# Optimization experiments

Measured on AMD Instinct MI355X. Metric: run time of the kernel, lower is better.

The kernel has to match this reference:

```python
import jax, jax.numpy as jnp
import numpy as np

B, N, K, OUT = 8, 2048, 30, 13


def _knn_idx(x, k):
    # x: [B,N,F] -> indices of k nearest neighbors (squared L2, includes self)
    sq = jnp.sum(x * x, axis=-1)  # [B,N]
    d = sq[:, :, None] + sq[:, None, :] - 2.0 * jnp.einsum('bnf,bmf->bnm', x, x)
    _, idx = jax.lax.top_k(-d, k)  # [B,N,k]
    return idx


def _edge_conv(x, W1, b1, g, be, W2, b2, k):
    # DynamicEdgeConv: kNN on feature space, message = MLP([x_i, x_j - x_i]), max aggr
    idx = _knn_idx(x, k)                                  # [B,N,k] (non-differentiable)
    xj = jax.vmap(lambda xb, ib: xb[ib])(x, idx)          # gather neighbors [B,N,k,F]
    xi = x[:, :, None, :]
    e = jnp.concatenate([jnp.broadcast_to(xi, xj.shape), xj - xi], axis=-1)  # [B,N,k,2F]
    # PyG MLP([2F,64,64]): Linear + BN(eval: affine) + ReLU, then plain Linear
    h = jax.nn.relu((e @ W1 + b1) * g + be)
    h = h @ W2 + b2
    return jnp.max(h, axis=2)                             # max over k neighbors -> [B,N,64]


def setup_inputs():
    key = jax.random.key(0)
    ks = jax.random.split(key, 40)

    def lin(i, fin, fout):
        W = jax.random.normal(ks[i], (fin, fout), jnp.float32) / np.sqrt(fin)
        return W, jnp.zeros((fout,), jnp.float32)

    inp = {}
    inp['x'] = jax.random.normal(ks[0], (B, N, 3), jnp.float32)
    inp['pos'] = jax.random.normal(ks[1], (B, N, 3), jnp.float32)
    inp['batch'] = jnp.repeat(jnp.arange(B, dtype=jnp.int32), N)
    i = 2
    for name, fin in [('c1', 12), ('c2', 128), ('c3', 128)]:
        W1, b1 = lin(i, fin, 64); i += 1
        W2, b2 = lin(i, 64, 64); i += 1
        inp[name + '_W1'] = W1; inp[name + '_b1'] = b1
        inp[name + '_g'] = 1.0 + 0.1 * jax.random.normal(ks[i], (64,), jnp.float32); i += 1
        inp[name + '_be'] = 0.1 * jax.random.normal(ks[i], (64,), jnp.float32); i += 1
        inp[name + '_W2'] = W2; inp[name + '_b2'] = b2
    dims = [192, 1024, 256, 128, OUT]
    for j in range(4):
        W, b = lin(i, dims[j], dims[j + 1]); i += 1
        inp[f'm_W{j + 1}'] = W; inp[f'm_b{j + 1}'] = b
    return inp


def reference(x, pos, batch,
              c1_W1, c1_b1, c1_g, c1_be, c1_W2, c1_b2,
              c2_W1, c2_b1, c2_g, c2_be, c2_W2, c2_b2,
              c3_W1, c3_b1, c3_g, c3_be, c3_W2, c3_b2,
              m_W1, m_b1, m_W2, m_b2, m_W3, m_b3, m_W4, m_b4):
    x0 = jnp.concatenate([pos, x], axis=-1)               # [B,N,6]
    x1 = _edge_conv(x0, c1_W1, c1_b1, c1_g, c1_be, c1_W2, c1_b2, K)
    x2 = _edge_conv(x1, c2_W1, c2_b1, c2_g, c2_be, c2_W2, c2_b2, K)
    x3 = _edge_conv(x2, c3_W1, c3_b1, c3_g, c3_be, c3_W2, c3_b2, K)
    h = jnp.concatenate([x1, x2, x3], axis=-1)            # [B,N,192]
    # classifier MLP([192,1024,256,128,OUT], norm=None): Linear+ReLU(+dropout=eval id), plain last
    h = jax.nn.relu(h @ m_W1 + m_b1)
    h = jax.nn.relu(h @ m_W2 + m_b2)
    h = jax.nn.relu(h @ m_W3 + m_b3)
    out = h @ m_W4 + m_b4
    return jax.nn.log_softmax(out, axis=-1), x3
```

## Files before the change

### kernel.cpp

```cpp
#include <hip/hip_runtime.h>

using u16 = unsigned short;
using u32 = unsigned int;
typedef short s8v __attribute__((ext_vector_type(8)));
typedef short s4v __attribute__((ext_vector_type(4)));
typedef float f4v __attribute__((ext_vector_type(4)));

#define DEV static __device__ __forceinline__

DEV void cvt_split(float f, u16& h, u16& l) {
  u32 x = __builtin_bit_cast(u32, f);
  u32 rh = (x + 0x7FFFu + ((x >> 16) & 1u)) & 0xFFFF0000u;
  h = (u16)(rh >> 16);
  float fl = f - __builtin_bit_cast(float, rh);
  u32 y = __builtin_bit_cast(u32, fl);
  l = (u16)((y + 0x7FFFu + ((y >> 16) & 1u)) >> 16);
}

__global__ void k_splitw(const float* __restrict__ W, int K, int N, int PK,
                         u16* __restrict__ Wh, u16* __restrict__ Wl) {
  int e = blockIdx.x * 256 + threadIdx.x;
  if (e >= K * N) return;
  int k = e / N, n = e % N;
  u16 h, l;
  cvt_split(W[e], h, l);
  Wh[(size_t)n * PK + k] = h;
  Wl[(size_t)n * PK + k] = l;
}

__global__ void k_build_x0(const float* __restrict__ x, const float* __restrict__ pos,
                           float* __restrict__ x0) {
  int p = blockIdx.x * 256 + threadIdx.x;
  float* o = x0 + (size_t)p * 8;
  o[0] = pos[p*3+0]; o[1] = pos[p*3+1]; o[2] = pos[p*3+2];
  o[3] = x[p*3+0];   o[4] = x[p*3+1];   o[5] = x[p*3+2];
  o[6] = 0.f; o[7] = 0.f;
}

__global__ void k_sqnorm(const float* __restrict__ x, int stride, int F,
                         float* __restrict__ sq) {
  int wid  = (blockIdx.x * 256 + threadIdx.x) >> 6;
  int lane = threadIdx.x & 63;
  float v = (lane < F) ? x[(size_t)wid * stride + lane] : 0.f;
  float s = v * v;
  #pragma unroll
  for (int m = 32; m; m >>= 1) s += __shfl_xor(s, m);
  if (lane == 0) sq[wid] = s;
}

template<int F>
__global__ __launch_bounds__(256) void k_dist(const float* __restrict__ x, int stride,
    const float* __restrict__ sq, int cbase, float* __restrict__ D) {
  constexpr int PAD = F + 4;
  __shared__ __align__(16) float Xi[128 * PAD];
  __shared__ __align__(16) float Xj[128 * PAD];
  __shared__ float SQI[128], SQJ[128];
  int b  = blockIdx.z;
  int i0 = cbase + blockIdx.y * 128;
  int j0 = blockIdx.x * 128;
  int tid = threadIdx.x;
  constexpr int NPASS = 128 * (F / 4) / 256;
  #pragma unroll
  for (int ps = 0; ps < NPASS; ++ps) {
    int e4 = ps * 256 + tid;
    int r = e4 / (F / 4), f4 = (e4 % (F / 4)) * 4;
    *(float4*)&Xi[r*PAD + f4] = *(const float4*)&x[(size_t)(b*2048 + i0 + r)*stride + f4];
    *(float4*)&Xj[r*PAD + f4] = *(const float4*)&x[(size_t)(b*2048 + j0 + r)*stride + f4];
  }
  if (tid < 128) {
    SQI[tid] = sq[b*2048 + i0 + tid];
    SQJ[tid] = sq[b*2048 + j0 + tid];
  }
  __syncthreads();
  int tx = tid & 15, ty = tid >> 4;
  float acc[8][8];
  #pragma unroll
  for (int i = 0; i < 8; ++i)
    #pragma unroll
    for (int j = 0; j < 8; ++j) acc[i][j] = 0.f;
  #pragma unroll 2
  for (int kf = 0; kf < F; kf += 4) {
    float4 av[8], wv[8];
    #pragma unroll
    for (int i = 0; i < 8; ++i) av[i] = *(const float4*)&Xi[(ty + 16*i)*PAD + kf];
    #pragma unroll
    for (int j = 0; j < 8; ++j) wv[j] = *(const float4*)&Xj[(tx + 16*j)*PAD + kf];
    #pragma unroll
    for (int i = 0; i < 8; ++i)
      #pragma unroll
      for (int j = 0; j < 8; ++j) {
        acc[i][j] += av[i].x * wv[j].x;
        acc[i][j] += av[i].y * wv[j].y;
        acc[i][j] += av[i].z * wv[j].z;
        acc[i][j] += av[i].w * wv[j].w;
      }
  }
  #pragma unroll
  for (int i = 0; i < 8; ++i) {
    int row = ty + 16*i;
    float si = SQI[row];
    #pragma unroll
    for (int j = 0; j < 8; ++j) {
      int col = tx + 16*j;
      D[(size_t)(b*512 + blockIdx.y*128 + row)*2048 + j0 + col] =
          si + SQJ[col] - 2.f * acc[i][j];
    }
  }
}

__global__ __launch_bounds__(256) void k_topk(const float* __restrict__ D, int cbase,
                                              int* __restrict__ knn) {
  int wid  = blockIdx.x * 4 + (threadIdx.x >> 6);
  int lane = threadIdx.x & 63;
  int b = wid >> 9, il = wid & 511;
  const float* row = D + (size_t)(b*512 + il) * 2048;
  float v[32];
  #pragma unroll
  for (int s = 0; s < 32; ++s) v[s] = row[lane + 64*s];
  const float INFV = __builtin_bit_cast(float, 0x7f800000u);
  int wj = 0;
  #pragma unroll 1
  for (int it = 0; it < 30; ++it) {
    float mv = v[0]; int ms = 0;
    #pragma unroll
    for (int s = 1; s < 32; ++s) {
      bool lt = v[s] < mv;
      mv = lt ? v[s] : mv;
      ms = lt ? s : ms;
    }
    int mj = lane + (ms << 6);
    #pragma unroll
    for (int m = 1; m < 64; m <<= 1) {
      float ov = __shfl_xor(mv, m);
      int   oj = __shfl_xor(mj, m);
      bool take = (ov < mv) || ((ov == mv) && (oj < mj));
      mv = take ? ov : mv;
      mj = take ? oj : mj;
    }
    int gj = __builtin_amdgcn_readfirstlane(mj);
    if (lane == it) wj = gj;
    int owner = gj & 63, slot = gj >> 6;
    #pragma unroll
    for (int s = 0; s < 32; ++s) {
      if (slot == s) {
        if (lane == owner) v[s] = INFV;
      }
    }
  }
  if (lane < 30) knn[(size_t)(b*2048 + cbase + il)*30 + lane] = b*2048 + wj;
}

__global__ __launch_bounds__(256) void k_prep(const float* __restrict__ x, int stride, int F,
    const float* __restrict__ W1, const float* __restrict__ b1,
    float* __restrict__ A0, float* __restrict__ V) {
  int p = blockIdx.x * 4 + (threadIdx.x >> 6);
  int lane = threadIdx.x & 63;
  float u = 0.f, v = 0.f;
  for (int f = 0; f < F; ++f) {
    float xv = x[(size_t)p*stride + f];
    float wa = W1[f*64 + lane];
    float wb = W1[(F + f)*64 + lane];
    u += xv * (wa - wb);
    v += xv * wb;
  }
  A0[p*64 + lane] = u + b1[lane];
  V[p*64 + lane]  = v;
}

__global__ __launch_bounds__(256) void k_edge_v(const float* __restrict__ A0,
    const float* __restrict__ V, const int* __restrict__ knn,
    const float* __restrict__ W2, const float* __restrict__ b2,
    const float* __restrict__ g, const float* __restrict__ be,
    float* __restrict__ out, int ostride) {
  int p = blockIdx.x * 4 + (threadIdx.x >> 6);
  int lane = threadIdx.x & 63;
  float w2c[64];
  #pragma unroll
  for (int c = 0; c < 64; ++c) w2c[c] = W2[c*64 + lane];
  float arow = A0[p*64 + lane];
  float gg = g[lane], bbe = be[lane];
  const int* kr = knn + p*30;
  float m = -3.0e38f;
  int j = kr[0];
  float vg = V[(size_t)j*64 + lane];
  #pragma unroll 1
  for (int k = 0; k < 30; ++k) {
    int jn = kr[k < 29 ? k + 1 : 29];
    float vgn = V[(size_t)jn*64 + lane];
    float pre = (arow + vg) * gg + bbe;
    float h1 = pre > 0.f ? pre : 0.f;
    u32 hb = __builtin_bit_cast(u32, h1);
    float s0 = 0.f, s1 = 0.f, s2 = 0.f, s3 = 0.f;
    #pragma unroll
    for (int c = 0; c < 64; c += 4) {
      s0 += __builtin_bit_cast(float, (u32)__builtin_amdgcn_readlane((int)hb, c+0)) * w2c[c+0];
      s1 += __builtin_bit_cast(float, (u32)__builtin_amdgcn_readlane((int)hb, c+1)) * w2c[c+1];
      s2 += __builtin_bit_cast(float, (u32)__builtin_amdgcn_readlane((int)hb, c+2)) * w2c[c+2];
      s3 += __builtin_bit_cast(float, (u32)__builtin_amdgcn_readlane((int)hb, c+3)) * w2c[c+3];
    }
    float h2 = (s0 + s1) + (s2 + s3);
    m = m > h2 ? m : h2;
    vg = vgn;
  }
  out[(size_t)p*ostride + lane] = m + b2[lane];
}

__global__ __launch_bounds__(256) void k_edge_m(const float* __restrict__ A0,
    const float* __restrict__ V, const int* __restrict__ knn,
    const u16* __restrict__ W2h, const u16* __restrict__ W2l,
    const float* __restrict__ b2,
    const float* __restrict__ g, const float* __restrict__ be,
    float* __restrict__ out, int ostride) {
  constexpr int PKW = 72;
  int p = blockIdx.x * 4 + (threadIdx.x >> 6);
  int lane = threadIdx.x & 63;
  int lr = lane & 15, kb = lane >> 4;

  const int* kr = knn + (size_t)p * 30;
  int j0 = kr[lr];
  int j1 = kr[lr + 16 < 30 ? lr + 16 : 29];

  s8v bh[4][2], bl[4][2];
  #pragma unroll
  for (int jf = 0; jf < 4; ++jf) {
    int n = jf*16 + lr;
    #pragma unroll
    for (int ks = 0; ks < 2; ++ks) {
      bh[jf][ks] = *(const s8v*)&W2h[n*PKW + ks*32 + kb*8];
      bl[jf][ks] = *(const s8v*)&W2l[n*PKW + ks*32 + kb*8];
    }
  }

  float base[2][8], gs[2][8];
  #pragma unroll
  for (int ks = 0; ks < 2; ++ks) {
    int cb = ks*32 + kb*8;
    float4 a0 = *(const float4*)&A0[(size_t)p*64 + cb];
    float4 a1 = *(const float4*)&A0[(size_t)p*64 + cb + 4];
    float4 g0 = *(const float4*)&g[cb];
    float4 g1 = *(const float4*)&g[cb + 4];
    float4 e0 = *(const float4*)&be[cb];
    float4 e1 = *(const float4*)&be[cb + 4];
    base[ks][0]=a0.x*g0.x+e0.x; base[ks][1]=a0.y*g0.y+e0.y;
    base[ks][2]=a0.z*g0.z+e0.z; base[ks][3]=a0.w*g0.w+e0.w;
    base[ks][4]=a1.x*g1.x+e1.x; base[ks][5]=a1.y*g1.y+e1.y;
    base[ks][6]=a1.z*g1.z+e1.z; base[ks][7]=a1.w*g1.w+e1.w;
    gs[ks][0]=g0.x; gs[ks][1]=g0.y; gs[ks][2]=g0.z; gs[ks][3]=g0.w;
    gs[ks][4]=g1.x; gs[ks][5]=g1.y; gs[ks][6]=g1.z; gs[ks][7]=g1.w;
  }

  s8v ah[2][2], al[2][2];
  #pragma unroll
  for (int mt = 0; mt < 2; ++mt) {
    const float* vr = V + (size_t)(mt ? j1 : j0) * 64;
    #pragma unroll
    for (int ks = 0; ks < 2; ++ks) {
      int cb = ks*32 + kb*8;
      float4 v0 = *(const float4*)&vr[cb];
      float4 v1 = *(const float4*)&vr[cb + 4];
      float hv[8];
      hv[0]=base[ks][0]+v0.x*gs[ks][0]; hv[1]=base[ks][1]+v0.y*gs[ks][1];
      hv[2]=base[ks][2]+v0.z*gs[ks][2]; hv[3]=base[ks][3]+v0.w*gs[ks][3];
      hv[4]=base[ks][4]+v1.x*gs[ks][4]; hv[5]=base[ks][5]+v1.y*gs[ks][5];
      hv[6]=base[ks][6]+v1.z*gs[ks][6]; hv[7]=base[ks][7]+v1.w*gs[ks][7];
      s8v hfrag, lfrag;
      #pragma unroll
      for (int e = 0; e < 8; ++e) {
        float h1 = hv[e] > 0.f ? hv[e] : 0.f;
        u16 hh, ll;
        cvt_split(h1, hh, ll);
        hfrag[e] = (short)hh; lfrag[e] = (short)ll;
      }
      ah[mt][ks] = hfrag; al[mt][ks] = lfrag;
    }
  }

  f4v acc[2][4];
  #pragma unroll
  for (int mt = 0; mt < 2; ++mt)
    #pragma unroll
    for (int jf = 0; jf < 4; ++jf) acc[mt][jf] = (f4v)(0.f);

  #pragma unroll
  for (int mt = 0; mt < 2; ++mt)
    #pragma unroll
    for (int jf = 0; jf < 4; ++jf)
      #pragma unroll
      for (int ks = 0; ks < 2; ++ks) {
        acc[mt][jf] = __builtin_amdgcn_mfma_f32_16x16x32_bf16(ah[mt][ks], bh[jf][ks], acc[mt][jf], 0, 0, 0);
        acc[mt][jf] = __builtin_amdgcn_mfma_f32_16x16x32_bf16(ah[mt][ks], bl[jf][ks], acc[mt][jf], 0, 0, 0);
        acc[mt][jf] = __builtin_amdgcn_mfma_f32_16x16x32_bf16(al[mt][ks], bh[jf][ks], acc[mt][jf], 0, 0, 0);
      }

  #pragma unroll
  for (int jf = 0; jf < 4; ++jf) {
    float m = fmaxf(fmaxf(acc[0][jf][0], acc[0][jf][1]), fmaxf(acc[0][jf][2], acc[0][jf][3]));
    float m1 = fmaxf(fmaxf(acc[1][jf][0], acc[1][jf][1]), fmaxf(acc[1][jf][2], acc[1][jf][3]));
    m = fmaxf(m, m1);
    m = fmaxf(m, __shfl_xor(m, 16));
    m = fmaxf(m, __shfl_xor(m, 32));
    if (kb == 0) out[(size_t)p*ostride + jf*16 + lr] = m + b2[jf*16 + lr];
  }
}

template<int NJF>
__global__ __launch_bounds__(256) void k_mlp(const float* __restrict__ Ag, int lda,
    const u16* __restrict__ Wth, const u16* __restrict__ Wtl, int PKW,
    const float* __restrict__ bg,
    float* __restrict__ Cg, int ldc, int N, int K, int dorelu) {
  constexpr int PK = 40;
  __shared__ __align__(16) u16 Ah[128*PK];
  __shared__ __align__(16) u16 Al[128*PK];
  int tid  = threadIdx.x;
  int wave = tid >> 6, lane = tid & 63;
  int wm = (wave >> 1) * 64, wn = (wave & 1) * (NJF*16);
  int lr = lane & 15, kb = lane >> 4;
  int m0 = blockIdx.y * 128, n0 = blockIdx.x * (2*NJF*16);

  f4v acc[4][NJF];
  #pragma unroll
  for (int i = 0; i < 4; ++i)
    #pragma unroll
    for (int j = 0; j < NJF; ++j) acc[i][j] = (f4v)(0.f);

  for (int k0 = 0; k0 < K; k0 += 32) {
    s8v bh[NJF], bl[NJF];
    #pragma unroll
    for (int jf = 0; jf < NJF; ++jf) {
      int n = n0 + wn + jf*16 + lr;
      bh[jf] = *(const s8v*)&Wth[(size_t)n*PKW + k0 + kb*8];
      bl[jf] = *(const s8v*)&Wtl[(size_t)n*PKW + k0 + kb*8];
    }
    #pragma unroll
    for (int ps = 0; ps < 4; ++ps) {
      int e4 = ps * 256 + tid;
      int r = e4 >> 3, c4 = (e4 & 7) << 2;
      float4 a = *(const float4*)&Ag[(size_t)(m0 + r)*lda + k0 + c4];
      u16 h0,h1,h2,h3,l0,l1,l2,l3;
      cvt_split(a.x, h0, l0); cvt_split(a.y, h1, l1);
      cvt_split(a.z, h2, l2); cvt_split(a.w, h3, l3);
      *(s4v*)&Ah[r*PK + c4] = s4v{(short)h0,(short)h1,(short)h2,(short)h3};
      *(s4v*)&Al[r*PK + c4] = s4v{(short)l0,(short)l1,(short)l2,(short)l3};
    }
    __syncthreads();
    #pragma unroll
    for (int mf = 0; mf < 4; ++mf) {
      int m = wm + mf*16 + lr;
      s8v ah = *(const s8v*)&Ah[m*PK + kb*8];
      s8v al = *(const s8v*)&Al[m*PK + kb*8];
      #pragma unroll
      for (int jf = 0; jf < NJF; ++jf) {
        acc[mf][jf] = __builtin_amdgcn_mfma_f32_16x16x32_bf16(ah, bh[jf], acc[mf][jf], 0, 0, 0);
        acc[mf][jf] = __builtin_amdgcn_mfma_f32_16x16x32_bf16(ah, bl[jf], acc[mf][jf], 0, 0, 0);
        acc[mf][jf] = __builtin_amdgcn_mfma_f32_16x16x32_bf16(al, bh[jf], acc[mf][jf], 0, 0, 0);
      }
    }
    __syncthreads();
  }

  #pragma unroll
  for (int jf = 0; jf < NJF; ++jf) {
    int n = n0 + wn + jf*16 + lr;
    float bb = bg[n];
    #pragma unroll
    for (int mf = 0; mf < 4; ++mf) {
      #pragma unroll
      for (int r = 0; r < 4; ++r) {
        int m = m0 + wm + mf*16 + kb*4 + r;
        float v = acc[mf][jf][r] + bb;
        if (dorelu) v = v > 0.f ? v : 0.f;
        Cg[(size_t)m*ldc + n] = v;
      }
    }
  }
}

__global__ __launch_bounds__(256) void k_head(const float* __restrict__ H3,
    const float* __restrict__ W4, const float* __restrict__ b4,
    float* __restrict__ out0, int pbase) {
  __shared__ float w4s[128 * 13];
  __shared__ float b4s[13];
  for (int e = threadIdx.x; e < 128*13; e += 256) w4s[e] = W4[e];
  if (threadIdx.x < 13) b4s[threadIdx.x] = b4[threadIdx.x];
  __syncthreads();
  int pl = blockIdx.x * 256 + threadIdx.x;
  float acc[13];
  #pragma unroll
  for (int c = 0; c < 13; ++c) acc[c] = b4s[c];
  const float* hr = H3 + (size_t)pl * 128;
  #pragma unroll 1
  for (int k = 0; k < 128; k += 4) {
    float4 h = *(const float4*)&hr[k];
    #pragma unroll
    for (int c = 0; c < 13; ++c) {
      acc[c] += h.x * w4s[(k+0)*13 + c];
      acc[c] += h.y * w4s[(k+1)*13 + c];
      acc[c] += h.z * w4s[(k+2)*13 + c];
      acc[c] += h.w * w4s[(k+3)*13 + c];
    }
  }
  float mx = acc[0];
  #pragma unroll
  for (int c = 1; c < 13; ++c) mx = fmaxf(mx, acc[c]);
  float s = 0.f;
  #pragma unroll
  for (int c = 0; c < 13; ++c) s += expf(acc[c] - mx);
  float lg = logf(s);
  size_t ob = (size_t)(pbase + pl) * 13;
  #pragma unroll
  for (int c = 0; c < 13; ++c) out0[ob + c] = acc[c] - mx - lg;
}

__global__ void k_out1(const float* __restrict__ hcat, float* __restrict__ out1) {
  int e = blockIdx.x * 256 + threadIdx.x;
  int p = e >> 6, c = e & 63;
  out1[e] = hcat[(size_t)p*192 + 128 + c];
}

extern "C" void kernel_launch(void* const* d_in, const int* in_sizes, int n_in,
                              void* d_out, int out_size, void* d_ws, size_t ws_size,
                              hipStream_t stream) {
  (void)in_sizes; (void)n_in; (void)out_size; (void)ws_size;
  const float* x   = (const float*)d_in[0];
  const float* pos = (const float*)d_in[1];
  const float* cw[3][6];
  for (int c = 0; c < 3; ++c)
    for (int t = 0; t < 6; ++t)
      cw[c][t] = (const float*)d_in[3 + c*6 + t];
  const float *mW[4], *mb[4];
  for (int j = 0; j < 4; ++j) {
    mW[j] = (const float*)d_in[21 + 2*j];
    mb[j] = (const float*)d_in[22 + 2*j];
  }

  float* ws   = (float*)d_ws;
  float* x0   = ws;
  float* sq   = x0 + 131072;
  int*   knn  = (int*)(sq + 16384);
  float* A0   = (float*)(knn + 491520);
  float* V    = A0 + 1048576;
  float* hcat = V + 1048576;
  float* U    = hcat + 3145728;
  float* H2c  = U + 8388608;
  float* H3c  = H2c + 2097152;
  u16* eW2 = (u16*)(H3c + 1048576);
  u16* mwp = (u16*)A0;
  u16* m1h = mwp;            u16* m1l = m1h + 204800;
  u16* m2h = m1l + 204800;   u16* m2l = m2h + 264192;
  u16* m3h = m2l + 264192;   u16* m3l = m3h + 33792;

  float* out0 = (float*)d_out;
  float* out1 = out0 + 8*2048*13;

  k_build_x0<<<64, 256, 0, stream>>>(x, pos, x0);
  k_splitw<<<16, 256, 0, stream>>>(cw[2][4], 64, 64, 72, eW2, eW2 + 4608);

  for (int c = 0; c < 3; ++c) {
    const float* xin; int stride, F, Fsq;
    if (c == 0)      { xin = x0;        stride = 8;   F = 6;  Fsq = 8;  }
    else if (c == 1) { xin = hcat;      stride = 192; F = 64; Fsq = 64; }
    else             { xin = hcat + 64; stride = 192; F = 64; Fsq = 64; }
    k_sqnorm<<<4096, 256, 0, stream>>>(xin, stride, Fsq, sq);
    for (int ch = 0; ch < 4; ++ch) {
      if (c == 0) k_dist<8> <<<dim3(16,4,8), 256, 0, stream>>>(xin, stride, sq, ch*512, U);
      else        k_dist<64><<<dim3(16,4,8), 256, 0, stream>>>(xin, stride, sq, ch*512, U);
      k_topk<<<1024, 256, 0, stream>>>(U, ch*512, knn);
    }
    k_prep<<<4096, 256, 0, stream>>>(xin, stride, F, cw[c][0], cw[c][1], A0, V);
    if (c < 2)
      k_edge_v<<<4096, 256, 0, stream>>>(A0, V, knn, cw[c][4], cw[c][5],
                                         cw[c][2], cw[c][3], hcat + 64*c, 192);
    else
      k_edge_m<<<4096, 256, 0, stream>>>(A0, V, knn, eW2, eW2 + 4608,
                                         cw[c][5], cw[c][2], cw[c][3], hcat + 64*c, 192);
  }

  k_splitw<<<768,  256, 0, stream>>>(mW[0], 192,  1024, 200,  m1h, m1l);
  k_splitw<<<1024, 256, 0, stream>>>(mW[1], 1024, 256,  1032, m2h, m2l);
  k_splitw<<<128,  256, 0, stream>>>(mW[2], 256,  128,  264,  m3h, m3l);

  for (int ch = 0; ch < 2; ++ch) {
    const float* Ain = hcat + (size_t)ch * 8192 * 192;
    k_mlp<4><<<dim3(8,64), 256, 0, stream>>>(Ain, 192,  m1h, m1l, 200,  mb[0], U,   1024, 1024, 192,  1);
    k_mlp<2><<<dim3(4,64), 256, 0, stream>>>(U,   1024, m2h, m2l, 1032, mb[1], H2c, 256,  256,  1024, 1);
    k_mlp<2><<<dim3(2,64), 256, 0, stream>>>(H2c, 256,  m3h, m3l, 264,  mb[2], H3c, 128,  128,  256,  1);
    k_head<<<32, 256, 0, stream>>>(H3c, mW[3], mb[3], out0, ch*8192);
  }
  k_out1<<<4096, 256, 0, stream>>>(hcat, out1);
}
```

Baseline: 1.343 ms.

## Remap edge-conv layers to one lane per neighbor and merge weight-prep kernels

The fp32 edge kernel used for the first two edge-conv layers is restructured. It previously ran one wave per point with a readlane broadcast per channel; now each lane handles one (point, neighbor) pair. Each lane computes the full 64-wide hidden vector in registers, dots it against a transposed W2 read with uniform addresses, writes results to shared memory, and a second pass takes the max over neighbors. Separately, the small setup and weight-splitting launches are merged into two kernels to cut launch count. The new layout uses 64 float registers per thread plus about 66KB of shared memory per block, which may lower occupancy, and 2 of 32 lanes per half-wave do redundant work.

Result: slower. 1.411 ms (+5.1%).

```diff
diff --git a/kernel.cpp b/kernel.cpp
--- a/kernel.cpp
+++ b/kernel.cpp
@@ -17,24 +17,60 @@
   l = (u16)((y + 0x7FFFu + ((y >> 16) & 1u)) >> 16);
 }
 
-__global__ void k_splitw(const float* __restrict__ W, int K, int N, int PK,
-                         u16* __restrict__ Wh, u16* __restrict__ Wl) {
-  int e = blockIdx.x * 256 + threadIdx.x;
-  if (e >= K * N) return;
-  int k = e / N, n = e % N;
+__global__ void k_misc0(const float* __restrict__ x, const float* __restrict__ pos,
+                        float* __restrict__ x0,
+                        const float* __restrict__ W2c3, u16* __restrict__ eW2h, u16* __restrict__ eW2l,
+                        const float* __restrict__ W2c1, const float* __restrict__ W2c2,
+                        float* __restrict__ W2T1, float* __restrict__ W2T2) {
+  int b = blockIdx.x;
+  if (b < 64) {
+    int p = b * 256 + threadIdx.x;
+    float* o = x0 + (size_t)p * 8;
+    o[0] = pos[p*3+0]; o[1] = pos[p*3+1]; o[2] = pos[p*3+2];
+    o[3] = x[p*3+0];   o[4] = x[p*3+1];   o[5] = x[p*3+2];
+    o[6] = 0.f; o[7] = 0.f;
+  } else if (b < 80) {
+    int e = (b - 64) * 256 + threadIdx.x;
+    int k = e >> 6, n = e & 63;
+    u16 h, l;
+    cvt_split(W2c3[e], h, l);
+    eW2h[n*72 + k] = h;
+    eW2l[n*72 + k] = l;
+  } else {
+    const float* src = (b == 80) ? W2c1 : W2c2;
+    float* dst = (b == 80) ? W2T1 : W2T2;
+    for (int e = threadIdx.x; e < 4096; e += 256) {
+      int c = e >> 6, cp = e & 63;
+      dst[cp*64 + c] = src[e];
+    }
+  }
+}
+
+__global__ void k_splitmlp(const float* __restrict__ W1, const float* __restrict__ W2,
+                           const float* __restrict__ W3,
+                           u16* __restrict__ m1h, u16* __restrict__ m1l,
+                           u16* __restrict__ m2h, u16* __restrict__ m2l,
+                           u16* __restrict__ m3h, u16* __restrict__ m3l) {
+  int b = blockIdx.x;
   u16 h, l;
-  cvt_split(W[e], h, l);
-  Wh[(size_t)n * PK + k] = h;
-  Wl[(size_t)n * PK + k] = l;
-}
-
-__global__ void k_build_x0(const float* __restrict__ x, const float* __restrict__ pos,
-                           float* __restrict__ x0) {
-  int p = blockIdx.x * 256 + threadIdx.x;
-  float* o = x0 + (size_t)p * 8;
-  o[0] = pos[p*3+0]; o[1] = pos[p*3+1]; o[2] = pos[p*3+2];
-  o[3] = x[p*3+0];   o[4] = x[p*3+1];   o[5] = x[p*3+2];
-  o[6] = 0.f; o[7] = 0.f;
+  if (b < 768) {
+    int e = b * 256 + threadIdx.x;
+    if (e < 192 * 1024) {
+      int k = e >> 10, n = e & 1023;
+      cvt_split(W1[e], h, l);
+      m1h[(size_t)n*200 + k] = h; m1l[(size_t)n*200 + k] = l;
+    }
+  } else if (b < 1792) {
+    int e = (b - 768) * 256 + threadIdx.x;
+    int k = e >> 8, n = e & 255;
+    cvt_split(W2[e], h, l);
+    m2h[(size_t)n*1032 + k] = h; m2l[(size_t)n*1032 + k] = l;
+  } else {
+    int e = (b - 1792) * 256 + threadIdx.x;
+    int k = e >> 7, n = e & 127;
+    cvt_split(W3[e], h, l);
+    m3h[(size_t)n*264 + k] = h; m3l[(size_t)n*264 + k] = l;
+  }
 }
 
 __global__ void k_sqnorm(const float* __restrict__ x, int stride, int F,
@@ -167,42 +203,49 @@
   V[p*64 + lane]  = v;
 }
 
-__global__ __launch_bounds__(256) void k_edge_v(const float* __restrict__ A0,
+__global__ __launch_bounds__(256) void k_edge_w(const float* __restrict__ A0,
     const float* __restrict__ V, const int* __restrict__ knn,
-    const float* __restrict__ W2, const float* __restrict__ b2,
+    const float* __restrict__ W2T, const float* __restrict__ b2,
     const float* __restrict__ g, const float* __restrict__ be,
     float* __restrict__ out, int ostride) {
-  int p = blockIdx.x * 4 + (threadIdx.x >> 6);
-  int lane = threadIdx.x & 63;
-  float w2c[64];
-  #pragma unroll
-  for (int c = 0; c < 64; ++c) w2c[c] = W2[c*64 + lane];
-  float arow = A0[p*64 + lane];
-  float gg = g[lane], bbe = be[lane];
-  const int* kr = knn + p*30;
-  float m = -3.0e38f;
-  int j = kr[0];
-  float vg = V[(size_t)j*64 + lane];
+  __shared__ float h2s[8][32][65];
+  int wave = threadIdx.x >> 6, lane = threadIdx.x & 63;
+  int half = lane >> 5, k = lane & 31;
+  int kk = k < 30 ? k : 29;
+  int pl = wave * 2 + half;
+  int p  = blockIdx.x * 8 + pl;
+  int j  = knn[(size_t)p * 30 + kk];
+
+  float h1[64];
+  const float* vr  = V  + (size_t)j * 64;
+  const float* a0r = A0 + (size_t)p * 64;
+  #pragma unroll
+  for (int c = 0; c < 64; ++c) {
+    float pre = (a0r[c] + vr[c]) * g[c] + be[c];
+    h1[c] = pre > 0.f ? pre : 0.f;
+  }
   #pragma unroll 1
-  for (int k = 0; k < 30; ++k) {
-    int jn = kr[k < 29 ? k + 1 : 29];
-    float vgn = V[(size_t)jn*64 + lane];
-    float pre = (arow + vg) * gg + bbe;
-    float h1 = pre > 0.f ? pre : 0.f;
-    u32 hb = __builtin_bit_cast(u32, h1);
+  for (int cp = 0; cp < 64; ++cp) {
+    const float* w = W2T + cp * 64;
     float s0 = 0.f, s1 = 0.f, s2 = 0.f, s3 = 0.f;
     #pragma unroll
     for (int c = 0; c < 64; c += 4) {
-      s0 += __builtin_bit_cast(float, (u32)__builtin_amdgcn_readlane((int)hb, c+0)) * w2c[c+0];
-      s1 += __builtin_bit_cast(float, (u32)__builtin_amdgcn_readlane((int)hb, c+1)) * w2c[c+1];
-      s2 += __builtin_bit_cast(float, (u32)__builtin_amdgcn_readlane((int)hb, c+2)) * w2c[c+2];
-      s3 += __builtin_bit_cast(float, (u32)__builtin_amdgcn_readlane((int)hb, c+3)) * w2c[c+3];
-    }
-    float h2 = (s0 + s1) + (s2 + s3);
-    m = m > h2 ? m : h2;
-    vg = vgn;
-  }
-  out[(size_t)p*ostride + lane] = m + b2[lane];
+      s0 += h1[c+0] * w[c+0];
+      s1 += h1[c+1] * w[c+1];
+      s2 += h1[c+2] * w[c+2];
+      s3 += h1[c+3] * w[c+3];
+    }
+    h2s[pl][k][cp] = (s0 + s1) + (s2 + s3);
+  }
+  __syncthreads();
+  #pragma unroll
+  for (int hh = 0; hh < 2; ++hh) {
+    int pp = wave * 2 + hh;
+    float m = h2s[pp][0][lane];
+    #pragma unroll
+    for (int t = 1; t < 30; ++t) m = fmaxf(m, h2s[pp][t][lane]);
+    out[(size_t)(blockIdx.x * 8 + pp) * ostride + lane] = m + b2[lane];
+  }
 }
 
 __global__ __launch_bounds__(256) void k_edge_m(const float* __restrict__ A0,
@@ -443,7 +486,9 @@
   float* U    = hcat + 3145728;
   float* H2c  = U + 8388608;
   float* H3c  = H2c + 2097152;
-  u16* eW2 = (u16*)(H3c + 1048576);
+  float* W2T1 = H3c + 1048576;
+  float* W2T2 = W2T1 + 4096;
+  u16*   eW2  = (u16*)(W2T2 + 4096);
   u16* mwp = (u16*)A0;
   u16* m1h = mwp;            u16* m1l = m1h + 204800;
   u16* m2h = m1l + 204800;   u16* m2l = m2h + 264192;
@@ -452,8 +497,8 @@
   float* out0 = (float*)d_out;
   float* out1 = out0 + 8*2048*13;
 
-  k_build_x0<<<64, 256, 0, stream>>>(x, pos, x0);
-  k_splitw<<<16, 256, 0, stream>>>(cw[2][4], 64, 64, 72, eW2, eW2 + 4608);
+  k_misc0<<<82, 256, 0, stream>>>(x, pos, x0, cw[2][4], eW2, eW2 + 4608,
+                                  cw[0][4], cw[1][4], W2T1, W2T2);
 
   for (int c = 0; c < 3; ++c) {
     const float* xin; int stride, F, Fsq;
@@ -468,16 +513,14 @@
     }
     k_prep<<<4096, 256, 0, stream>>>(xin, stride, F, cw[c][0], cw[c][1], A0, V);
     if (c < 2)
-      k_edge_v<<<4096, 256, 0, stream>>>(A0, V, knn, cw[c][4], cw[c][5],
-                                         cw[c][2], cw[c][3], hcat + 64*c, 192);
+      k_edge_w<<<2048, 256, 0, stream>>>(A0, V, knn, c == 0 ? W2T1 : W2T2,
+                                         cw[c][5], cw[c][2], cw[c][3], hcat + 64*c, 192);
     else
       k_edge_m<<<4096, 256, 0, stream>>>(A0, V, knn, eW2, eW2 + 4608,
                                          cw[c][5], cw[c][2], cw[c][3], hcat + 64*c, 192);
   }
 
-  k_splitw<<<768,  256, 0, stream>>>(mW[0], 192,  1024, 200,  m1h, m1l);
-  k_splitw<<<1024, 256, 0, stream>>>(mW[1], 1024, 256,  1032, m2h, m2l);
-  k_splitw<<<128,  256, 0, stream>>>(mW[2], 256,  128,  264,  m3h, m3l);
+  k_splitmlp<<<1920, 256, 0, stream>>>(mW[0], mW[1], mW[2], m1h, m1l, m2h, m2l, m3h, m3l);
 
   for (int ch = 0; ch < 2; ++ch) {
     const float* Ain = hcat + (size_t)ch * 8192 * 192;
```
